# Optimization experiments

Hardware: AMD Instinct MI355X
Metric: run time of the kernel (lower is better)

The kernel has to match this reference:

```python
import jax, jax.numpy as jnp
import numpy as np

N = 500000        # total atoms (n1 nodes)
G = 20000         # graphs (g nodes)
D_IN = 128        # in_features
D_H = 256         # hidden width (config_local / mid_features)
D_OUT = 1         # final output per graph (config_global last int)


def setup_inputs() -> dict:
    key = jax.random.key(0)
    ks = jax.random.split(key, 10)
    h = jax.random.normal(ks[0], (N, D_IN), dtype=jnp.float32)
    graph_ids = jnp.sort(jax.random.randint(ks[1], (N,), 0, G))
    s = 0.05
    return {
        "h": h,
        "graph_ids": graph_ids,
        "num_graphs": G,
        # d_local: Linear(128->256) relu, Linear(256->256) relu
        "W1": jax.random.normal(ks[2], (D_IN, D_H), dtype=jnp.float32) * s,
        "b1": jnp.zeros((D_H,), dtype=jnp.float32),
        "W2": jax.random.normal(ks[3], (D_H, D_H), dtype=jnp.float32) * s,
        "b2": jnp.zeros((D_H,), dtype=jnp.float32),
        # d_global: Linear(256->256) relu, Linear(256->1)
        "Wg1": jax.random.normal(ks[4], (D_H, D_H), dtype=jnp.float32) * s,
        "bg1": jnp.zeros((D_H,), dtype=jnp.float32),
        "Wg2": jax.random.normal(ks[5], (D_H, D_OUT), dtype=jnp.float32) * s,
        "bg2": jnp.zeros((D_OUT,), dtype=jnp.float32),
    }


def reference(h, graph_ids, num_graphs, W1, b1, W2, b2, Wg1, bg1, Wg2, bg2):
    # node-level MLP (d_local): h_global per n1 node
    x = jax.nn.relu(h @ W1 + b1)            # [N, D_H]
    x = jax.nn.relu(x @ W2 + b2)            # [N, D_H]
    # copy_src + sum over n1_in_g edges == per-graph segment sum
    pooled = jax.ops.segment_sum(x, graph_ids, num_segments=num_graphs)  # [G, D_H]
    # graph-level MLP (d_global)
    y = jax.nn.relu(pooled @ Wg1 + bg1)     # [G, D_H]
    return y @ Wg2 + bg2                    # [G, 1]
```

## Files before the change

### kernel.cpp

```cpp
#include <hip/hip_runtime.h>
#include <stdint.h>

#define D_IN 128
#define D_H  256
#define BM   64

typedef float f32x4 __attribute__((ext_vector_type(4)));
typedef short s16x8 __attribute__((ext_vector_type(8)));
typedef unsigned int u32x2 __attribute__((ext_vector_type(2)));
typedef unsigned int u32x4 __attribute__((ext_vector_type(4)));

__device__ __forceinline__ unsigned short f2bf(float x) {
  union { float f; uint32_t u; } v; v.f = x;
  uint32_t r = v.u + 0x7fffu + ((v.u >> 16) & 1u);
  return (unsigned short)(r >> 16);
}
__device__ __forceinline__ float bf2f(unsigned short u) {
  union { uint32_t u; float f; } v; v.u = (uint32_t)u << 16;
  return v.f;
}

__global__ void prep_kernel(const float* __restrict__ W1, const float* __restrict__ W2,
                            const float* __restrict__ Wg1,
                            float* __restrict__ pooled, unsigned short* __restrict__ W1t,
                            unsigned short* __restrict__ W2t, unsigned short* __restrict__ Wg1t,
                            int pooled_n) {
  int stride = gridDim.x * blockDim.x;
  int tid = blockIdx.x * blockDim.x + threadIdx.x;
  for (int i = tid; i < pooled_n; i += stride) pooled[i] = 0.0f;
  for (int i = tid; i < D_H * D_IN; i += stride) {
    int n = i >> 7, k = i & (D_IN - 1);
    W1t[i] = f2bf(W1[k * D_H + n]);
  }
  for (int i = tid; i < D_H * D_H; i += stride) {
    int n = i >> 8, k = i & (D_H - 1);
    W2t[i]  = f2bf(W2[k * D_H + n]);
    Wg1t[i] = f2bf(Wg1[k * D_H + n]);
  }
}


__global__ __launch_bounds__(256, 3)
void node_kernel(const float* __restrict__ h, const int* __restrict__ gids,
                 const float* __restrict__ b1, const float* __restrict__ b2,
                 const unsigned short* __restrict__ W1t, const unsigned short* __restrict__ W2t,
                 float* __restrict__ pooled, int nnodes) {
  __shared__ unsigned short hA[BM * D_IN];
  __shared__ unsigned short x1s[BM * D_H];
  __shared__ int sgid[BM];
  const int tid  = threadIdx.x;
  const int lane = tid & 63;
  const int wave = tid >> 6;
  const int lr   = lane & 15;
  const int q    = lane >> 4;
  const int row0 = blockIdx.x * BM;

  s16x8 a[4][4];
  #pragma unroll
  for (int ks = 0; ks < 4; ++ks)
    #pragma unroll
    for (int mt = 0; mt < 4; ++mt)
      a[ks][mt] = *(const s16x8*)&W1t[(wave * 64 + mt * 16 + lr) * D_IN + ks * 32 + q * 8];

  if (tid < BM) {
    int gr = row0 + tid;
    sgid[tid] = (gr < nnodes) ? gids[gr] : -1;
  }

  #pragma unroll
  for (int i = 0; i < 4; ++i) {
    int gi = tid + i * 256;
    int r  = gi >> 4;
    int gc = gi & 15;
    int gr = row0 + r;
    f32x4 v0 = (f32x4){0.f, 0.f, 0.f, 0.f}, v1 = v0;
    if (gr < nnodes) {
      const f32x4* p = (const f32x4*)(h + (size_t)gr * D_IN + gc * 8);
      v0 = __builtin_nontemporal_load(p);
      v1 = __builtin_nontemporal_load(p + 1);
    }
    u32x4 u;
    u[0] = f2bf(v0[0]) | ((uint32_t)f2bf(v0[1]) << 16);
    u[1] = f2bf(v0[2]) | ((uint32_t)f2bf(v0[3]) << 16);
    u[2] = f2bf(v1[0]) | ((uint32_t)f2bf(v1[1]) << 16);
    u[3] = f2bf(v1[2]) | ((uint32_t)f2bf(v1[3]) << 16);
    *(u32x4*)&hA[r * D_IN + ((gc ^ (r & 7)) << 3)] = u;
  }
  __syncthreads();

  f32x4 acc[4][4];
  #pragma unroll
  for (int mt = 0; mt < 4; ++mt)
    #pragma unroll
    for (int nt = 0; nt < 4; ++nt)
      acc[mt][nt] = (f32x4){0.f, 0.f, 0.f, 0.f};

  #pragma unroll
  for (int ks = 0; ks < 4; ++ks) {
    const int kq = ks * 32 + q * 8;
    s16x8 b[4];
    #pragma unroll
    for (int nt = 0; nt < 4; ++nt)
      b[nt] = *(const s16x8*)&hA[(nt * 16 + lr) * D_IN + (((kq >> 3) ^ (lr & 7)) << 3)];
    #pragma unroll
    for (int mt = 0; mt < 4; ++mt)
      #pragma unroll
      for (int nt = 0; nt < 4; ++nt)
        acc[mt][nt] = __builtin_amdgcn_mfma_f32_16x16x32_bf16(a[ks][mt], b[nt], acc[mt][nt], 0, 0, 0);
  }

  #pragma unroll
  for (int mt = 0; mt < 4; ++mt) {
    int f = wave * 64 + mt * 16 + q * 4;
    float4 bias = *(const float4*)&b1[f];
    #pragma unroll
    for (int nt = 0; nt < 4; ++nt) {
      int nd = nt * 16 + lr;
      uint32_t p0 = f2bf(fmaxf(acc[mt][nt][0] + bias.x, 0.f)) |
                    ((uint32_t)f2bf(fmaxf(acc[mt][nt][1] + bias.y, 0.f)) << 16);
      uint32_t p1 = f2bf(fmaxf(acc[mt][nt][2] + bias.z, 0.f)) |
                    ((uint32_t)f2bf(fmaxf(acc[mt][nt][3] + bias.w, 0.f)) << 16);
      u32x2 w = {p0, p1};
      *(u32x2*)&x1s[nd * D_H + (((f >> 3) ^ (nd & 7)) << 3) + (f & 7)] = w;
    }
  }

  #pragma unroll
  for (int ks = 0; ks < 4; ++ks)
    #pragma unroll
    for (int mt = 0; mt < 4; ++mt)
      a[ks][mt] = *(const s16x8*)&W2t[(wave * 64 + mt * 16 + lr) * D_H + ks * 32 + q * 8];
  __syncthreads();

  #pragma unroll
  for (int mt = 0; mt < 4; ++mt)
    #pragma unroll
    for (int nt = 0; nt < 4; ++nt)
      acc[mt][nt] = (f32x4){0.f, 0.f, 0.f, 0.f};

  #pragma unroll
  for (int ks = 0; ks < 4; ++ks) {
    const int kq = ks * 32 + q * 8;
    s16x8 b[4];
    #pragma unroll
    for (int nt = 0; nt < 4; ++nt)
      b[nt] = *(const s16x8*)&x1s[(nt * 16 + lr) * D_H + (((kq >> 3) ^ (lr & 7)) << 3)];
    #pragma unroll
    for (int mt = 0; mt < 4; ++mt)
      #pragma unroll
      for (int nt = 0; nt < 4; ++nt)
        acc[mt][nt] = __builtin_amdgcn_mfma_f32_16x16x32_bf16(a[ks][mt], b[nt], acc[mt][nt], 0, 0, 0);
  }
  #pragma unroll
  for (int ks = 0; ks < 4; ++ks)
    #pragma unroll
    for (int mt = 0; mt < 4; ++mt)
      a[ks][mt] = *(const s16x8*)&W2t[(wave * 64 + mt * 16 + lr) * D_H + 128 + ks * 32 + q * 8];
  #pragma unroll
  for (int ks = 0; ks < 4; ++ks) {
    const int kq = 128 + ks * 32 + q * 8;
    s16x8 b[4];
    #pragma unroll
    for (int nt = 0; nt < 4; ++nt)
      b[nt] = *(const s16x8*)&x1s[(nt * 16 + lr) * D_H + (((kq >> 3) ^ (lr & 7)) << 3)];
    #pragma unroll
    for (int mt = 0; mt < 4; ++mt)
      #pragma unroll
      for (int nt = 0; nt < 4; ++nt)
        acc[mt][nt] = __builtin_amdgcn_mfma_f32_16x16x32_bf16(a[ks][mt], b[nt], acc[mt][nt], 0, 0, 0);
  }
  __syncthreads();

  #pragma unroll
  for (int mt = 0; mt < 4; ++mt) {
    int f = wave * 64 + mt * 16 + q * 4;
    float4 bias = *(const float4*)&b2[f];
    #pragma unroll
    for (int nt = 0; nt < 4; ++nt) {
      int nd = nt * 16 + lr;
      uint32_t p0 = f2bf(fmaxf(acc[mt][nt][0] + bias.x, 0.f)) |
                    ((uint32_t)f2bf(fmaxf(acc[mt][nt][1] + bias.y, 0.f)) << 16);
      uint32_t p1 = f2bf(fmaxf(acc[mt][nt][2] + bias.z, 0.f)) |
                    ((uint32_t)f2bf(fmaxf(acc[mt][nt][3] + bias.w, 0.f)) << 16);
      u32x2 w = {p0, p1};
      *(u32x2*)&x1s[nd * D_H + (((f >> 3) ^ (nd & 7)) << 3) + (f & 7)] = w;
    }
  }
  __syncthreads();

  float racc = 0.f;
  for (int r = 0; r < BM; ++r) {
    int g = sgid[r];
    if (g >= 0) {
      racc += bf2f(x1s[r * D_H + (((tid >> 3) ^ (r & 7)) << 3) + (tid & 7)]);
      if (r == BM - 1 || sgid[r + 1] != g) {
        atomicAdd(&pooled[g * D_H + tid], racc);
        racc = 0.f;
      }
    }
  }
}

union GraphSmem {
  unsigned short pA[BM][D_H + 8];
  float y[BM][D_H + 4];
};

__global__ __launch_bounds__(256, 2)
void graph_kernel(const float* __restrict__ pooled, const float* __restrict__ bg1,
                  const unsigned short* __restrict__ Wg1t, const float* __restrict__ Wg2,
                  const float* __restrict__ bg2, float* __restrict__ out, int ngraphs) {
  __shared__ GraphSmem sm;
  const int tid  = threadIdx.x;
  const int lane = tid & 63;
  const int wave = tid >> 6;
  const int lr   = lane & 15;
  const int q    = lane >> 4;
  const int g0   = blockIdx.x * BM;

  #pragma unroll
  for (int i = 0; i < 16; ++i) {
    int f4 = tid + i * 256;
    int r  = f4 >> 6;
    int c4 = f4 & 63;
    float4 v = make_float4(0.f, 0.f, 0.f, 0.f);
    if (g0 + r < ngraphs) v = ((const float4*)pooled)[(size_t)(g0 + r) * 64 + c4];
    uint32_t p0 = f2bf(v.x) | ((uint32_t)f2bf(v.y) << 16);
    uint32_t p1 = f2bf(v.z) | ((uint32_t)f2bf(v.w) << 16);
    uint32_t* dst = (uint32_t*)&sm.pA[r][c4 * 4];
    dst[0] = p0; dst[1] = p1;
  }
  __syncthreads();

  f32x4 acc[4][4];
  #pragma unroll
  for (int mt = 0; mt < 4; ++mt)
    #pragma unroll
    for (int nt = 0; nt < 4; ++nt)
      acc[mt][nt] = (f32x4){0.f, 0.f, 0.f, 0.f};

  #pragma unroll
  for (int kk = 0; kk < D_H; kk += 32) {
    const int kq = kk + q * 8;
    s16x8 a[4], b[4];
    #pragma unroll
    for (int mt = 0; mt < 4; ++mt) {
      int f = wave * 64 + mt * 16 + lr;
      a[mt] = *(const s16x8*)&Wg1t[f * D_H + kq];
    }
    #pragma unroll
    for (int nt = 0; nt < 4; ++nt)
      b[nt] = *(const s16x8*)&sm.pA[nt * 16 + lr][kq];
    #pragma unroll
    for (int mt = 0; mt < 4; ++mt)
      #pragma unroll
      for (int nt = 0; nt < 4; ++nt)
        acc[mt][nt] = __builtin_amdgcn_mfma_f32_16x16x32_bf16(a[mt], b[nt], acc[mt][nt], 0, 0, 0);
  }
  __syncthreads();

  #pragma unroll
  for (int mt = 0; mt < 4; ++mt) {
    int f = wave * 64 + mt * 16 + q * 4;
    float4 bias = *(const float4*)&bg1[f];
    #pragma unroll
    for (int nt = 0; nt < 4; ++nt) {
      int nd = nt * 16 + lr;
      f32x4 v;
      v[0] = fmaxf(acc[mt][nt][0] + bias.x, 0.f);
      v[1] = fmaxf(acc[mt][nt][1] + bias.y, 0.f);
      v[2] = fmaxf(acc[mt][nt][2] + bias.z, 0.f);
      v[3] = fmaxf(acc[mt][nt][3] + bias.w, 0.f);
      *(f32x4*)&sm.y[nd][f] = v;
    }
  }
  __syncthreads();

  int gloc = tid >> 2;
  int part = tid & 3;
  float p = 0.f;
  #pragma unroll 8
  for (int i = 0; i < 64; ++i) {
    int f = part + 4 * i;
    p += sm.y[gloc][f] * Wg2[f];
  }
  p += __shfl_xor(p, 1);
  p += __shfl_xor(p, 2);
  if (part == 0 && (g0 + gloc) < ngraphs)
    out[g0 + gloc] = p + bg2[0];
}

extern "C" void kernel_launch(void* const* d_in, const int* in_sizes, int n_in,
                              void* d_out, int out_size, void* d_ws, size_t ws_size,
                              hipStream_t stream) {
  const float* h   = (const float*)d_in[0];
  const int*   gid = (const int*)d_in[1];
  const float* W1  = (const float*)d_in[3];
  const float* b1  = (const float*)d_in[4];
  const float* W2  = (const float*)d_in[5];
  const float* b2  = (const float*)d_in[6];
  const float* Wg1 = (const float*)d_in[7];
  const float* bg1 = (const float*)d_in[8];
  const float* Wg2 = (const float*)d_in[9];
  const float* bg2 = (const float*)d_in[10];
  float* out = (float*)d_out;

  const int N = in_sizes[1];
  const int G = out_size;

  char* ws = (char*)d_ws;
  float* pooled = (float*)ws;
  size_t off = (size_t)G * D_H * sizeof(float);
  unsigned short* W1t  = (unsigned short*)(ws + off); off += (size_t)D_H * D_IN * 2;
  unsigned short* W2t  = (unsigned short*)(ws + off); off += (size_t)D_H * D_H * 2;
  unsigned short* Wg1t = (unsigned short*)(ws + off);

  prep_kernel<<<512, 256, 0, stream>>>(W1, W2, Wg1, pooled, W1t, W2t, Wg1t, G * D_H);
  node_kernel<<<(N + BM - 1) / BM, 256, 0, stream>>>(h, gid, b1, b2, W1t, W2t, pooled, N);
  graph_kernel<<<(G + BM - 1) / BM, 256, 0, stream>>>(pooled, bg1, Wg1t, Wg2, bg2, out, G);
}
```

Baseline: 579.3 us.

## Shrink shared memory, use packed bf16 converts, and raise graph kernel occupancy

The node kernel's two shared buffers become one, with the input tile aliased into the upper half of the activation buffer. It drops one barrier before pooling and hoists the W2 register loads ahead of a barrier so the first-layer activations can overwrite the aliased region. Packed bf16 conversion intrinsics replace the manual rounding, and pooled zeroing is vectorised. The graph kernel keeps its hidden activations in bf16 in a swizzled layout instead of fp32, cutting LDS use so launch bounds can rise to 4 blocks per CU, at some cost in precision for the final dot product.

```diff
diff --git a/kernel.cpp b/kernel.cpp
--- a/kernel.cpp
+++ b/kernel.cpp
@@ -18,6 +18,14 @@
 __device__ __forceinline__ float bf2f(unsigned short u) {
   union { uint32_t u; float f; } v; v.u = (uint32_t)u << 16;
   return v.f;
+}
+__device__ __forceinline__ uint32_t pkbf(float lo, float hi) {
+#if __has_builtin(__builtin_amdgcn_cvt_pk_bf16_f32)
+  auto r = __builtin_amdgcn_cvt_pk_bf16_f32(lo, hi);
+  uint32_t u; __builtin_memcpy(&u, &r, 4); return u;
+#else
+  return (uint32_t)f2bf(lo) | ((uint32_t)f2bf(hi) << 16);
+#endif
 }
 
 __global__ void prep_kernel(const float* __restrict__ W1, const float* __restrict__ W2,
@@ -27,7 +35,8 @@
                             int pooled_n) {
   int stride = gridDim.x * blockDim.x;
   int tid = blockIdx.x * blockDim.x + threadIdx.x;
-  for (int i = tid; i < pooled_n; i += stride) pooled[i] = 0.0f;
+  float4 z4 = make_float4(0.f, 0.f, 0.f, 0.f);
+  for (int i = tid; i < (pooled_n >> 2); i += stride) ((float4*)pooled)[i] = z4;
   for (int i = tid; i < D_H * D_IN; i += stride) {
     int n = i >> 7, k = i & (D_IN - 1);
     W1t[i] = f2bf(W1[k * D_H + n]);
@@ -38,15 +47,13 @@
     Wg1t[i] = f2bf(Wg1[k * D_H + n]);
   }
 }
-
 
 __global__ __launch_bounds__(256, 3)
 void node_kernel(const float* __restrict__ h, const int* __restrict__ gids,
                  const float* __restrict__ b1, const float* __restrict__ b2,
                  const unsigned short* __restrict__ W1t, const unsigned short* __restrict__ W2t,
                  float* __restrict__ pooled, int nnodes) {
-  __shared__ unsigned short hA[BM * D_IN];
-  __shared__ unsigned short x1s[BM * D_H];
+  __shared__ unsigned short buf[BM * D_H];
   __shared__ int sgid[BM];
   const int tid  = threadIdx.x;
   const int lane = tid & 63;
@@ -54,6 +61,7 @@
   const int lr   = lane & 15;
   const int q    = lane >> 4;
   const int row0 = blockIdx.x * BM;
+  unsigned short* hA = buf + 8192;
 
   s16x8 a[4][4];
   #pragma unroll
@@ -69,10 +77,7 @@
 
   #pragma unroll
   for (int i = 0; i < 4; ++i) {
-    int gi = tid + i * 256;
-    int r  = gi >> 4;
-    int gc = gi & 15;
-    int gr = row0 + r;
+    int gi = tid + i * 256, r = gi >> 4, gc = gi & 15, gr = row0 + r;
     f32x4 v0 = (f32x4){0.f, 0.f, 0.f, 0.f}, v1 = v0;
     if (gr < nnodes) {
       const f32x4* p = (const f32x4*)(h + (size_t)gr * D_IN + gc * 8);
@@ -80,10 +85,8 @@
       v1 = __builtin_nontemporal_load(p + 1);
     }
     u32x4 u;
-    u[0] = f2bf(v0[0]) | ((uint32_t)f2bf(v0[1]) << 16);
-    u[1] = f2bf(v0[2]) | ((uint32_t)f2bf(v0[3]) << 16);
-    u[2] = f2bf(v1[0]) | ((uint32_t)f2bf(v1[1]) << 16);
-    u[3] = f2bf(v1[2]) | ((uint32_t)f2bf(v1[3]) << 16);
+    u[0] = pkbf(v0[0], v0[1]); u[1] = pkbf(v0[2], v0[3]);
+    u[2] = pkbf(v1[0], v1[1]); u[3] = pkbf(v1[2], v1[3]);
     *(u32x4*)&hA[r * D_IN + ((gc ^ (r & 7)) << 3)] = u;
   }
   __syncthreads();
@@ -110,26 +113,26 @@
   }
 
   #pragma unroll
+  for (int ks = 0; ks < 4; ++ks)
+    #pragma unroll
+    for (int mt = 0; mt < 4; ++mt)
+      a[ks][mt] = *(const s16x8*)&W2t[(wave * 64 + mt * 16 + lr) * D_H + ks * 32 + q * 8];
+
+  __syncthreads();
+
+  #pragma unroll
   for (int mt = 0; mt < 4; ++mt) {
     int f = wave * 64 + mt * 16 + q * 4;
     float4 bias = *(const float4*)&b1[f];
     #pragma unroll
     for (int nt = 0; nt < 4; ++nt) {
       int nd = nt * 16 + lr;
-      uint32_t p0 = f2bf(fmaxf(acc[mt][nt][0] + bias.x, 0.f)) |
-                    ((uint32_t)f2bf(fmaxf(acc[mt][nt][1] + bias.y, 0.f)) << 16);
-      uint32_t p1 = f2bf(fmaxf(acc[mt][nt][2] + bias.z, 0.f)) |
-                    ((uint32_t)f2bf(fmaxf(acc[mt][nt][3] + bias.w, 0.f)) << 16);
-      u32x2 w = {p0, p1};
-      *(u32x2*)&x1s[nd * D_H + (((f >> 3) ^ (nd & 7)) << 3) + (f & 7)] = w;
-    }
-  }
-
-  #pragma unroll
-  for (int ks = 0; ks < 4; ++ks)
-    #pragma unroll
-    for (int mt = 0; mt < 4; ++mt)
-      a[ks][mt] = *(const s16x8*)&W2t[(wave * 64 + mt * 16 + lr) * D_H + ks * 32 + q * 8];
+      u32x2 w;
+      w[0] = pkbf(fmaxf(acc[mt][nt][0] + bias.x, 0.f), fmaxf(acc[mt][nt][1] + bias.y, 0.f));
+      w[1] = pkbf(fmaxf(acc[mt][nt][2] + bias.z, 0.f), fmaxf(acc[mt][nt][3] + bias.w, 0.f));
+      *(u32x2*)&buf[nd * D_H + (((f >> 3) ^ (nd & 7)) << 3) + (f & 7)] = w;
+    }
+  }
   __syncthreads();
 
   #pragma unroll
@@ -144,7 +147,7 @@
     s16x8 b[4];
     #pragma unroll
     for (int nt = 0; nt < 4; ++nt)
-      b[nt] = *(const s16x8*)&x1s[(nt * 16 + lr) * D_H + (((kq >> 3) ^ (lr & 7)) << 3)];
+      b[nt] = *(const s16x8*)&buf[(nt * 16 + lr) * D_H + (((kq >> 3) ^ (lr & 7)) << 3)];
     #pragma unroll
     for (int mt = 0; mt < 4; ++mt)
       #pragma unroll
@@ -162,7 +165,7 @@
     s16x8 b[4];
     #pragma unroll
     for (int nt = 0; nt < 4; ++nt)
-      b[nt] = *(const s16x8*)&x1s[(nt * 16 + lr) * D_H + (((kq >> 3) ^ (lr & 7)) << 3)];
+      b[nt] = *(const s16x8*)&buf[(nt * 16 + lr) * D_H + (((kq >> 3) ^ (lr & 7)) << 3)];
     #pragma unroll
     for (int mt = 0; mt < 4; ++mt)
       #pragma unroll
@@ -178,39 +181,34 @@
     #pragma unroll
     for (int nt = 0; nt < 4; ++nt) {
       int nd = nt * 16 + lr;
-      uint32_t p0 = f2bf(fmaxf(acc[mt][nt][0] + bias.x, 0.f)) |
-                    ((uint32_t)f2bf(fmaxf(acc[mt][nt][1] + bias.y, 0.f)) << 16);
-      uint32_t p1 = f2bf(fmaxf(acc[mt][nt][2] + bias.z, 0.f)) |
-                    ((uint32_t)f2bf(fmaxf(acc[mt][nt][3] + bias.w, 0.f)) << 16);
-      u32x2 w = {p0, p1};
-      *(u32x2*)&x1s[nd * D_H + (((f >> 3) ^ (nd & 7)) << 3) + (f & 7)] = w;
-    }
-  }
-  __syncthreads();
-
-  float racc = 0.f;
-  for (int r = 0; r < BM; ++r) {
-    int g = sgid[r];
-    if (g >= 0) {
-      racc += bf2f(x1s[r * D_H + (((tid >> 3) ^ (r & 7)) << 3) + (tid & 7)]);
-      if (r == BM - 1 || sgid[r + 1] != g) {
-        atomicAdd(&pooled[g * D_H + tid], racc);
-        racc = 0.f;
+      u32x2 w;
+      w[0] = pkbf(fmaxf(acc[mt][nt][0] + bias.x, 0.f), fmaxf(acc[mt][nt][1] + bias.y, 0.f));
+      w[1] = pkbf(fmaxf(acc[mt][nt][2] + bias.z, 0.f), fmaxf(acc[mt][nt][3] + bias.w, 0.f));
+      *(u32x2*)&buf[nd * D_H + (((f >> 3) ^ (nd & 7)) << 3) + (f & 7)] = w;
+    }
+  }
+
+  {
+    const int hi = tid >> 3, lo = tid & 7;
+    float racc = 0.f;
+    for (int r = 0; r < BM; ++r) {
+      int g = sgid[r];
+      if (g >= 0) {
+        racc += bf2f(buf[r * D_H + ((hi ^ (r & 7)) << 3) + lo]);
+        if (r == BM - 1 || sgid[r + 1] != g) {
+          atomicAdd(&pooled[g * D_H + tid], racc);
+          racc = 0.f;
+        }
       }
     }
   }
 }
 
-union GraphSmem {
-  unsigned short pA[BM][D_H + 8];
-  float y[BM][D_H + 4];
-};
-
-__global__ __launch_bounds__(256, 2)
+__global__ __launch_bounds__(256, 4)
 void graph_kernel(const float* __restrict__ pooled, const float* __restrict__ bg1,
                   const unsigned short* __restrict__ Wg1t, const float* __restrict__ Wg2,
                   const float* __restrict__ bg2, float* __restrict__ out, int ngraphs) {
-  __shared__ GraphSmem sm;
+  __shared__ unsigned short pA[BM * D_H];
   const int tid  = threadIdx.x;
   const int lane = tid & 63;
   const int wave = tid >> 6;
@@ -219,16 +217,18 @@
   const int g0   = blockIdx.x * BM;
 
   #pragma unroll
-  for (int i = 0; i < 16; ++i) {
-    int f4 = tid + i * 256;
-    int r  = f4 >> 6;
-    int c4 = f4 & 63;
-    float4 v = make_float4(0.f, 0.f, 0.f, 0.f);
-    if (g0 + r < ngraphs) v = ((const float4*)pooled)[(size_t)(g0 + r) * 64 + c4];
-    uint32_t p0 = f2bf(v.x) | ((uint32_t)f2bf(v.y) << 16);
-    uint32_t p1 = f2bf(v.z) | ((uint32_t)f2bf(v.w) << 16);
-    uint32_t* dst = (uint32_t*)&sm.pA[r][c4 * 4];
-    dst[0] = p0; dst[1] = p1;
+  for (int i = 0; i < 8; ++i) {
+    int gi = tid + i * 256, r = gi >> 5, gc = gi & 31;
+    int gr = g0 + r;
+    f32x4 v0 = (f32x4){0.f, 0.f, 0.f, 0.f}, v1 = v0;
+    if (gr < ngraphs) {
+      const f32x4* p = (const f32x4*)(pooled + (size_t)gr * D_H + gc * 8);
+      v0 = p[0]; v1 = p[1];
+    }
+    u32x4 u;
+    u[0] = pkbf(v0[0], v0[1]); u[1] = pkbf(v0[2], v0[3]);
+    u[2] = pkbf(v1[0], v1[1]); u[3] = pkbf(v1[2], v1[3]);
+    *(u32x4*)&pA[r * D_H + (((gc & 7) ^ (r & 7)) << 3) + ((gc & 24) << 3)] = u;
   }
   __syncthreads();
 
@@ -240,17 +240,17 @@
       acc[mt][nt] = (f32x4){0.f, 0.f, 0.f, 0.f};
 
   #pragma unroll
-  for (int kk = 0; kk < D_H; kk += 32) {
-    const int kq = kk + q * 8;
+  for (int ks = 0; ks < 8; ++ks) {
+    const int kq = ks * 32 + q * 8;
     s16x8 a[4], b[4];
     #pragma unroll
-    for (int mt = 0; mt < 4; ++mt) {
-      int f = wave * 64 + mt * 16 + lr;
-      a[mt] = *(const s16x8*)&Wg1t[f * D_H + kq];
-    }
-    #pragma unroll
-    for (int nt = 0; nt < 4; ++nt)
-      b[nt] = *(const s16x8*)&sm.pA[nt * 16 + lr][kq];
+    for (int mt = 0; mt < 4; ++mt)
+      a[mt] = *(const s16x8*)&Wg1t[(wave * 64 + mt * 16 + lr) * D_H + kq];
+    #pragma unroll
+    for (int nt = 0; nt < 4; ++nt) {
+      int row = nt * 16 + lr, gw = kq >> 3;
+      b[nt] = *(const s16x8*)&pA[row * D_H + (((gw & 7) ^ (row & 7)) << 3) + ((gw & 24) << 3)];
+    }
     #pragma unroll
     for (int mt = 0; mt < 4; ++mt)
       #pragma unroll
@@ -266,12 +266,11 @@
     #pragma unroll
     for (int nt = 0; nt < 4; ++nt) {
       int nd = nt * 16 + lr;
-      f32x4 v;
-      v[0] = fmaxf(acc[mt][nt][0] + bias.x, 0.f);
-      v[1] = fmaxf(acc[mt][nt][1] + bias.y, 0.f);
-      v[2] = fmaxf(acc[mt][nt][2] + bias.z, 0.f);
-      v[3] = fmaxf(acc[mt][nt][3] + bias.w, 0.f);
-      *(f32x4*)&sm.y[nd][f] = v;
+      u32x2 w;
+      w[0] = pkbf(fmaxf(acc[mt][nt][0] + bias.x, 0.f), fmaxf(acc[mt][nt][1] + bias.y, 0.f));
+      w[1] = pkbf(fmaxf(acc[mt][nt][2] + bias.z, 0.f), fmaxf(acc[mt][nt][3] + bias.w, 0.f));
+      int gw = f >> 3;
+      *(u32x2*)&pA[nd * D_H + (((gw & 7) ^ (nd & 7)) << 3) + ((gw & 24) << 3) + (f & 7)] = w;
     }
   }
   __syncthreads();
@@ -280,9 +279,15 @@
   int part = tid & 3;
   float p = 0.f;
   #pragma unroll 8
-  for (int i = 0; i < 64; ++i) {
-    int f = part + 4 * i;
-    p += sm.y[gloc][f] * Wg2[f];
+  for (int i = 0; i < 32; ++i) {
+    int f2 = part + 4 * i;
+    int hw = 2 * f2;
+    int gw = hw >> 3;
+    uint32_t wv = *(const uint32_t*)&pA[gloc * D_H + (((gw & 7) ^ (gloc & 7)) << 3) +
+                                        ((gw & 24) << 3) + (hw & 7)];
+    float2 wg = ((const float2*)Wg2)[f2];
+    p += bf2f((unsigned short)(wv & 0xffffu)) * wg.x +
+         bf2f((unsigned short)(wv >> 16)) * wg.y;
   }
   p += __shfl_xor(p, 1);
   p += __shfl_xor(p, 2);
```

Result: no change. 573.2 us (-1.1%).
